# Kernel optimization log

Hardware: AMD Instinct MI355X
Metric: run time of the kernel (lower is better)

## Reference

```python
import math
import jax
import jax.numpy as jnp
import numpy as np

MUL = 32            # multiplicity of 0e and 1o in irreps_in/out
N_NODES = 50000
N_EDGES = 800000
N_BASIS = 10
N_HID = 100
NUM_NEIGHBORS = 16.0


def setup_inputs() -> dict:
    key = jax.random.key(0)
    ks = jax.random.split(key, 14)
    return {
        "node_input": jax.random.normal(ks[0], (N_NODES, 4 * MUL), jnp.float32),
        "node_attr": jnp.ones((N_NODES, 1), jnp.float32),
        "edge_src": jax.random.randint(ks[1], (N_EDGES,), 0, N_NODES, dtype=jnp.int32),
        "edge_dst": jax.random.randint(ks[2], (N_EDGES,), 0, N_NODES, dtype=jnp.int32),
        "edge_attr": jax.random.normal(ks[3], (N_EDGES, 4), jnp.float32),
        "edge_length_embedded": jax.random.uniform(ks[4], (N_EDGES, N_BASIS), dtype=jnp.float32),
        "W_sc0": jax.random.normal(ks[5], (MUL, MUL), jnp.float32),
        "W_sc1": jax.random.normal(ks[6], (MUL, MUL), jnp.float32),
        "W_l10": jax.random.normal(ks[7], (MUL, MUL), jnp.float32),
        "W_l11": jax.random.normal(ks[8], (MUL, MUL), jnp.float32),
        "W_l20": jax.random.normal(ks[9], (2 * MUL, MUL), jnp.float32),
        "W_l21": jax.random.normal(ks[10], (2 * MUL, MUL), jnp.float32),
        "W_fc1": jax.random.normal(ks[11], (N_BASIS, N_HID), jnp.float32),
        "W_fc2": jax.random.normal(ks[12], (N_HID, 4 * MUL), jnp.float32),
    }


def _fctp(x0, x1, attr, W0, W1):
    """FullyConnectedTensorProduct with a 1x0e attr: per-irrep linear * scalar attr.
    x0: [N,U], x1: [N,U,3], attr: [N,1]. Path norm alpha = 1/sqrt(fan_in)."""
    inv = 1.0 / math.sqrt(W0.shape[0])
    o0 = attr * (x0 @ W0) * inv                                    # [N,W]
    o1 = attr[:, :, None] * jnp.einsum("nud,uw->nwd", x1, W1) * inv  # [N,W,3]
    return o0, o1


def _forward(node_input, node_attr, edge_attr, edge_length_embedded,
             W_sc0, W_sc1, W_l10, W_l11, W_l20, W_l21, W_fc1, W_fc2,
             edge_src, edge_dst):
    N = node_input.shape[0]
    x0 = node_input[:, :MUL]                       # [N,32]  0e
    x1 = node_input[:, MUL:].reshape(N, MUL, 3)    # [N,32,3] 1o

    # self-connection and lin1 (both attr is scalar 0e)
    s0, s1 = _fctp(x0, x1, node_attr, W_sc0, W_sc1)
    y0, y1 = _fctp(x0, x1, node_attr, W_l10, W_l11)

    # radial MLP -> per-edge uvu weights (weight_numel = 4*MUL)
    h = jax.nn.silu(edge_length_embedded @ W_fc1 * (1.0 / math.sqrt(N_BASIS)))
    w = h @ W_fc2 * (1.0 / math.sqrt(N_HID))       # [E,128]
    w1, w2, w3, w4 = (w[:, 0*MUL:1*MUL], w[:, 1*MUL:2*MUL],
                      w[:, 2*MUL:3*MUL], w[:, 3*MUL:4*MUL])

    # gather source node features per edge
    x0s = y0[edge_src]                              # [E,32]
    x1s = y1[edge_src]                              # [E,32,3]
    ea0 = edge_attr[:, :1]                          # [E,1]   0e
    ea1 = edge_attr[:, 1:]                          # [E,3]   1o

    # segmented uvu tensor product (CG for lmax=1, component norm)
    mid0a = w1 * x0s * ea0                                         # 0e x 0e -> 0e
    mid0b = w4 * jnp.einsum("eum,em->eu", x1s, ea1) * (1.0 / math.sqrt(3.0))  # 1o x 1o -> 0e
    mid1a = (w2 * x0s)[:, :, None] * ea1[:, None, :]               # 0e x 1o -> 1o
    mid1b = w3[:, :, None] * x1s * ea0[:, None, :]                 # 1o x 0e -> 1o
    E = edge_attr.shape[0]
    edge_features = jnp.concatenate(
        [mid0a, mid0b, mid1a.reshape(E, -1), mid1b.reshape(E, -1)], axis=1)  # [E,256]

    # scatter-add to destination nodes
    agg = jax.ops.segment_sum(edge_features, edge_dst, num_segments=N)
    agg = agg * (1.0 / math.sqrt(NUM_NEIGHBORS))

    m0 = agg[:, :2 * MUL]                           # [N,64]  0e part of irreps_mid
    m1 = agg[:, 2 * MUL:].reshape(N, 2 * MUL, 3)    # [N,64,3] 1o part
    z0, z1 = _fctp(m0, m1, node_attr, W_l20, W_l21)

    # sc output_mask is all ones (every output irrep reachable)
    c_s = math.sin(math.pi / 8.0)
    c_x = math.cos(math.pi / 8.0)
    out0 = c_s * s0 + c_x * z0
    out1 = c_s * s1 + c_x * z1
    return jnp.concatenate([out0, out1.reshape(N, -1)], axis=1)   # [N,128]


def reference(node_input, node_attr, edge_src, edge_dst, edge_attr, edge_length_embedded,
              W_sc0, W_sc1, W_l10, W_l11, W_l20, W_l21, W_fc1, W_fc2):
    return _forward(node_input, node_attr, edge_attr, edge_length_embedded,
                    W_sc0, W_sc1, W_l10, W_l11, W_l20, W_l21, W_fc1, W_fc2,
                    edge_src, edge_dst)
```

## Files before the change

kernel.cpp:

```cpp
#include <hip/hip_runtime.h>
#include <hip/hip_bf16.h>

#define MUL 32
#define F4 128
#define NB 10
#define NH 100
#define EROW 136
#define FROW 72
#define REC 48

#define INV_SQRT32 0.17677669529663687f
#define INV_SQRT10 0.31622776601683794f
#define INV_SQRT100 0.1f
#define INV_SQRT3 0.5773502691896258f
#define AGG_SCALE 0.25f
#define INV8 0.125f
#define C_S 0.3826834323650898f
#define C_X 0.9238795325112867f

typedef __attribute__((ext_vector_type(8))) short short8;
typedef __attribute__((ext_vector_type(4))) float float4v;

__device__ __forceinline__ float bf2f(__hip_bfloat16 v) { return __bfloat162float(v); }
__device__ __forceinline__ unsigned short f2b(float x) {
    __hip_bfloat16 b = __float2bfloat16(x);
    return *(unsigned short*)&b;
}
__device__ __forceinline__ float b2f(unsigned short u) {
    __hip_bfloat16 b;
    *(unsigned short*)&b = u;
    return __bfloat162float(b);
}
__device__ __forceinline__ float ldin(const void* p, size_t i, int f) {
    return f ? ((const float*)p)[i] : bf2f(((const __hip_bfloat16*)p)[i]);
}

__device__ __forceinline__ void barrier_lds() {
    asm volatile("s_waitcnt lgkmcnt(0)" ::: "memory");
    __builtin_amdgcn_s_barrier();
}

__global__ void detect_dtype_kernel(const void* __restrict__ node_attr, int* __restrict__ flag) {
    unsigned w = *(const unsigned*)node_attr;
    *flag = (w == 0x3F800000u) ? 1 : 0;
}

__global__ __launch_bounds__(256) void prep_kernel(
    const void* __restrict__ Wfc1,
    const void* __restrict__ Wfc2,
    const void* __restrict__ Wl20,
    const void* __restrict__ Wl21,
    const int* __restrict__ flagp,
    unsigned short* __restrict__ w1t,
    unsigned short* __restrict__ w2t,
    unsigned short* __restrict__ w20t,
    unsigned short* __restrict__ w21t)
{
    int f = *flagp;
    int gi = blockIdx.x * 256 + threadIdx.x;
    if (gi < 128 * 128) {
        int n = gi >> 7, k = gi & 127;
        w2t[gi] = (k < NH) ? f2b(ldin(Wfc2, (size_t)k * 128 + n, f)) : 0;
    }
    if (gi < 32 * 64) {
        int v = gi >> 6, u = gi & 63;
        w20t[gi] = f2b(ldin(Wl20, (size_t)u * 32 + v, f));
        w21t[gi] = f2b(ldin(Wl21, (size_t)u * 32 + v, f));
    }
    if (gi < 112 * 32) {
        int n = gi >> 5, k = gi & 31;
        w1t[gi] = (k < NB && n < NH) ? f2b(ldin(Wfc1, (size_t)k * NH + n, f)) : 0;
    }
}

__global__ __launch_bounds__(256) void hist_kernel(
    const int* __restrict__ edst, int* __restrict__ cnt, int E)
{
    int i = blockIdx.x * 256 + threadIdx.x;
    if (i < E) atomicAdd(&cnt[edst[i]], 1);
}

__global__ __launch_bounds__(1024) void scanA_kernel(
    int* __restrict__ cnt, int* __restrict__ bsum, int N)
{
    __shared__ int wsum[16];
    int t = threadIdx.x, lane = t & 63, wid = t >> 6;
    int i = blockIdx.x * 1024 + t;
    int v = (i < N) ? cnt[i] : 0;
    int x = v;
#pragma unroll
    for (int d = 1; d < 64; d <<= 1) { int yv = __shfl_up(x, d); if (lane >= d) x += yv; }
    if (lane == 63) wsum[wid] = x;
    __syncthreads();
    if (wid == 0 && lane < 16) {
        int s = wsum[lane];
#pragma unroll
        for (int d = 1; d < 16; d <<= 1) { int yv = __shfl_up(s, d); if (lane >= d) s += yv; }
        wsum[lane] = s;
    }
    __syncthreads();
    int pre = (wid > 0 ? wsum[wid - 1] : 0);
    if (i < N) cnt[i] = pre + x - v;
    if (t == 0) bsum[blockIdx.x] = wsum[15];
}

__global__ __launch_bounds__(64) void scanB_kernel(int* __restrict__ bsum, int nb)
{
    int t = threadIdx.x;
    int carry = 0;
    for (int c0 = 0; c0 < nb; c0 += 64) {
        int idx = c0 + t;
        int v = (idx < nb) ? bsum[idx] : 0;
        int x = v;
#pragma unroll
        for (int d = 1; d < 64; d <<= 1) { int yv = __shfl_up(x, d); if (t >= d) x += yv; }
        if (idx < nb) bsum[idx] = carry + x - v;
        carry += __shfl(x, 63);
    }
}

__global__ __launch_bounds__(1024) void scanC_kernel(
    int* __restrict__ cnt, const int* __restrict__ bsum, int N)
{
    int i = blockIdx.x * 1024 + threadIdx.x;
    if (i < N) cnt[i] += bsum[blockIdx.x];
}

__global__ __launch_bounds__(256) void scatter_build_kernel(
    const int* __restrict__ edst,
    const int* __restrict__ esrc,
    const void* __restrict__ eattr,
    const void* __restrict__ ele,
    const int* __restrict__ flagp,
    int* __restrict__ cnt,
    unsigned char* __restrict__ rec, int E)
{
    int i = blockIdx.x * 256 + threadIdx.x;
    if (i >= E) return;
    int f = *flagp;
    int d = edst[i];
    int p = atomicAdd(&cnt[d], 1);

    unsigned e0 = f2b(ldin(ele, (size_t)i * NB + 0, f));
    unsigned e1 = f2b(ldin(ele, (size_t)i * NB + 1, f));
    unsigned e2 = f2b(ldin(ele, (size_t)i * NB + 2, f));
    unsigned e3 = f2b(ldin(ele, (size_t)i * NB + 3, f));
    unsigned e4 = f2b(ldin(ele, (size_t)i * NB + 4, f));
    unsigned e5 = f2b(ldin(ele, (size_t)i * NB + 5, f));
    unsigned e6 = f2b(ldin(ele, (size_t)i * NB + 6, f));
    unsigned e7 = f2b(ldin(ele, (size_t)i * NB + 7, f));
    unsigned e8 = f2b(ldin(ele, (size_t)i * NB + 8, f));
    unsigned e9 = f2b(ldin(ele, (size_t)i * NB + 9, f));
    float ea0 = ldin(eattr, (size_t)i * 4 + 0, f);
    float ea1 = ldin(eattr, (size_t)i * 4 + 1, f);
    float ea2 = ldin(eattr, (size_t)i * 4 + 2, f);
    float ea3 = ldin(eattr, (size_t)i * 4 + 3, f);

    unsigned char* r = rec + (size_t)p * REC;
    *(int4*)(r + 0)  = make_int4(esrc[i], d, (int)(e0 | (e1 << 16)), (int)(e2 | (e3 << 16)));
    *(int4*)(r + 16) = make_int4((int)(e4 | (e5 << 16)), (int)(e6 | (e7 << 16)), (int)(e8 | (e9 << 16)), 0);
    *(float4*)(r + 32) = make_float4(ea0, ea1, ea2, ea3);
}

__global__ __launch_bounds__(256) void node_y_kernel(
    const void* __restrict__ node_input,
    const void* __restrict__ node_attr,
    const void* __restrict__ Wl10,
    const void* __restrict__ Wl11,
    const int* __restrict__ flagp,
    unsigned short* __restrict__ y, int N)
{
    __shared__ float sW0[1024];
    __shared__ float sW1[1024];
    __shared__ float sX[16 * 128];
    int f = *flagp;
    int t = threadIdx.x;
    for (int i = t; i < 1024; i += 256) {
        sW0[i] = ldin(Wl10, i, f);
        sW1[i] = ldin(Wl11, i, f);
    }
    int n0 = blockIdx.x * 16;
    for (int i = t; i < 2048; i += 256) {
        int ln = i >> 7, c = i & 127, n = n0 + ln;
        sX[i] = (n < N) ? ldin(node_input, (size_t)n * F4 + c, f) : 0.f;
    }
    __syncthreads();
    for (int i = t; i < 2048; i += 256) {
        int ln = i >> 7, c = i & 127, n = n0 + ln;
        if (n >= N) continue;
        float attr = ldin(node_attr, n, f);
        float acc = 0.f;
        if (c < 32) {
#pragma unroll
            for (int u = 0; u < 32; u++) acc += sX[ln * 128 + u] * sW0[u * 32 + c];
        } else {
            int d = (c - 32) >> 5, u0 = (c - 32) & 31;
#pragma unroll
            for (int u = 0; u < 32; u++) acc += sX[ln * 128 + 32 + u * 3 + d] * sW1[u * 32 + u0];
        }
        y[(size_t)n * F4 + c] = f2b(acc * attr * INV_SQRT32);
    }
}

#define SM_ELEB  0
#define SM_HW    4096
#define SM_DST   21504
#define SM_TOTAL 21760

__global__ __launch_bounds__(256, 6) void fused_edge_kernel(
    const unsigned char* __restrict__ rec,
    const unsigned short* __restrict__ y,
    const unsigned short* __restrict__ w1t,
    const unsigned short* __restrict__ w2t,
    const unsigned short* __restrict__ w20t,
    const unsigned short* __restrict__ w21t,
    float* __restrict__ agg,
    int E)
{
    __shared__ __align__(16) char smem[SM_TOTAL];
    unsigned short* sEleB = (unsigned short*)(smem + SM_ELEB);
    unsigned short* sHW = (unsigned short*)(smem + SM_HW);
    int* sDst = (int*)(smem + SM_DST);

    int t = threadIdx.x;
    int base = blockIdx.x * 64;
    int ne = E - base;
    if (ne > 64) ne = 64;

    int w = t >> 6, lane = t & 63;
    int lm = lane & 15, quad = lane >> 4;
    int em = w * 16 + lm;

    int src = (em < ne) ? *(const int*)(rec + (size_t)(base + em) * REC) : 0;
    float4 ea4 = (em < ne) ? *(const float4*)(rec + (size_t)(base + em) * REC + 32)
                           : make_float4(0.f, 0.f, 0.f, 0.f);
    const unsigned short* yrg = y + (size_t)src * 128;
    short8 x0  = *(const short8*)(yrg + quad * 8);
    short8 xd0 = *(const short8*)(yrg + 32 + quad * 8);
    short8 xd1 = *(const short8*)(yrg + 64 + quad * 8);
    short8 xd2 = *(const short8*)(yrg + 96 + quad * 8);
    short8 w1f[7];
#pragma unroll
    for (int nt = 0; nt < 7; nt++)
        w1f[nt] = *(const short8*)(w1t + (nt * 16 + lm) * 32 + quad * 8);

    if (t < 64)
        sDst[t] = (t < ne) ? *(const int*)(rec + (size_t)(base + t) * REC + 4) : -1;
    for (int i = t; i < 64 * 32; i += 256) {
        int e = i >> 5, k = i & 31;
        unsigned short v = 0;
        if (k < NB && e < ne)
            v = *(const unsigned short*)(rec + (size_t)(base + e) * REC + 8 + 2 * k);
        sEleB[i] = v;
    }
    barrier_lds();

    {
        short8 a = *(const short8*)(sEleB + (w * 16 + lm) * 32 + quad * 8);
#pragma unroll
        for (int nt = 0; nt < 7; nt++) {
            float4v c1 = (float4v){0.f, 0.f, 0.f, 0.f};
            c1 = __builtin_amdgcn_mfma_f32_16x16x32_bf16(a, w1f[nt], c1, 0, 0, 0);
            int ch = nt * 16 + lm;
#pragma unroll
            for (int r = 0; r < 4; r++) {
                int row = w * 16 + quad * 4 + r;
                float hv = 0.f;
                if (ch < NH) {
                    float aa = c1[r] * INV_SQRT10;
                    hv = aa / (1.f + __expf(-aa));
                }
                sHW[row * EROW + ch] = f2b(hv);
            }
        }
        int e = t >> 2, seg = t & 3;
        *(uint2*)(sHW + e * EROW + 112 + seg * 4) = (uint2){0u, 0u};
    }
    barrier_lds();

    short8 hfr[4];
#pragma unroll
    for (int kc = 0; kc < 4; kc++)
        hfr[kc] = *(const short8*)(sHW + (w * 16 + lm) * EROW + kc * 32 + quad * 8);
    barrier_lds();
#pragma unroll
    for (int nt = 0; nt < 8; nt++) {
        float4v c2 = (float4v){0.f, 0.f, 0.f, 0.f};
#pragma unroll
        for (int kc = 0; kc < 4; kc++) {
            short8 b = *(const short8*)(w2t + (nt * 16 + lm) * 128 + kc * 32 + quad * 8);
            c2 = __builtin_amdgcn_mfma_f32_16x16x32_bf16(hfr[kc], b, c2, 0, 0, 0);
        }
#pragma unroll
        for (int r = 0; r < 4; r++)
            sHW[(w * 16 + quad * 4 + r) * EROW + nt * 16 + lm] = f2b(c2[r] * INV_SQRT100);
    }
    barrier_lds();

    {
        const unsigned short* wr = sHW + em * EROW;
        short8 wA = *(const short8*)(wr + quad * 8);
        short8 wB = *(const short8*)(wr + 32 + quad * 8);
        short8 wC = *(const short8*)(wr + 64 + quad * 8);
        short8 wD = *(const short8*)(wr + 96 + quad * 8);
        float ea0 = ea4.x;
        float e1x = ea4.y;
        float e1y = ea4.z;
        float e1z = ea4.w;
        float ea0S = ea0 * AGG_SCALE;
        float s3 = AGG_SCALE * INV_SQRT3;

        short8 f00, f01, f10, f11, f20, f21, f30, f31;
#pragma unroll
        for (int j = 0; j < 8; j++) {
            float x0f = b2f((unsigned short)x0[j]);
            float d0f = b2f((unsigned short)xd0[j]);
            float d1f = b2f((unsigned short)xd1[j]);
            float d2f = b2f((unsigned short)xd2[j]);
            f00[j] = (short)f2b(b2f((unsigned short)wA[j]) * x0f * ea0S);
            float tt = d0f * e1x + d1f * e1y + d2f * e1z;
            f01[j] = (short)f2b(b2f((unsigned short)wD[j]) * tt * s3);
            float p = b2f((unsigned short)wB[j]) * x0f * AGG_SCALE;
            f10[j] = (short)f2b(p * e1x);
            f20[j] = (short)f2b(p * e1y);
            f30[j] = (short)f2b(p * e1z);
            float q = b2f((unsigned short)wC[j]) * ea0S;
            f11[j] = (short)f2b(q * d0f);
            f21[j] = (short)f2b(q * d1f);
            f31[j] = (short)f2b(q * d2f);
        }

        barrier_lds();
        unsigned short* sFeatT = (unsigned short*)smem;
#pragma unroll
        for (int g = 0; g < 4; g++) {
            const unsigned short* wt = g ? w21t : w20t;
            short8 ak0 = (g == 0) ? f00 : (g == 1) ? f10 : (g == 2) ? f20 : f30;
            short8 ak1 = (g == 0) ? f01 : (g == 1) ? f11 : (g == 2) ? f21 : f31;
#pragma unroll
            for (int nt = 0; nt < 2; nt++) {
                float4v acc = (float4v){0.f, 0.f, 0.f, 0.f};
                short8 b0 = *(const short8*)(wt + (nt * 16 + lm) * 64 + quad * 8);
                short8 b1 = *(const short8*)(wt + (nt * 16 + lm) * 64 + 32 + quad * 8);
                acc = __builtin_amdgcn_mfma_f32_16x16x32_bf16(ak0, b0, acc, 0, 0, 0);
                acc = __builtin_amdgcn_mfma_f32_16x16x32_bf16(ak1, b1, acc, 0, 0, 0);
                int ch = (g == 0) ? (nt * 16 + lm) : (32 + (g - 1) * 32 + nt * 16 + lm);
                short4 sv;
                sv.x = (short)f2b(acc[0]);
                sv.y = (short)f2b(acc[1]);
                sv.z = (short)f2b(acc[2]);
                sv.w = (short)f2b(acc[3]);
                *(short4*)(sFeatT + ch * FROW + (w * 16 + quad * 4)) = sv;
            }
        }
        barrier_lds();

        if (t < 128) {
            int c = t;
            unsigned long long m =
                __ballot((lane == 0) ? 1 : (sDst[lane] != sDst[lane - 1]));
            const unsigned short* fr = sFeatT + c * FROW;
            short8 fv[8];
#pragma unroll
            for (int q8 = 0; q8 < 8; q8++)
                fv[q8] = *(const short8*)(fr + q8 * 8);
            float s = 0.f;
            int rs = 0;
#pragma unroll
            for (int e = 0; e < 64; e++) {
                s += b2f((unsigned short)fv[e >> 3][e & 7]);
                bool fl = (e == 63) || ((m >> (e + 1)) & 1ull);
                if (fl) {
                    int d = sDst[e];
                    if (d >= 0) {
                        if (rs > 0 && e < ne - 1) agg[(size_t)d * F4 + c] = s;
                        else atomicAdd(&agg[(size_t)d * F4 + c], s);
                    }
                    s = 0.f;
                    rs = e + 1;
                }
            }
        }
    }
}

__global__ __launch_bounds__(256) void out_kernel(
    const void* __restrict__ node_input,
    const void* __restrict__ node_attr,
    const void* __restrict__ Wsc0,
    const void* __restrict__ Wsc1,
    const float* __restrict__ agg,
    const int* __restrict__ flagp,
    void* __restrict__ out, int N)
{
    __shared__ float sWs0[1024], sWs1[1024];
    __shared__ float sX[16 * 128];
    __shared__ float sA[16 * 128];
    int f = *flagp;
    int t = threadIdx.x;
    for (int i = t; i < 1024; i += 256) {
        sWs0[i] = ldin(Wsc0, i, f);
        sWs1[i] = ldin(Wsc1, i, f);
    }
    int n0 = blockIdx.x * 16;
    for (int i = t; i < 2048; i += 256) {
        int ln = i >> 7, c = i & 127, n = n0 + ln;
        sX[i] = (n < N) ? ldin(node_input, (size_t)n * F4 + c, f) : 0.f;
        sA[i] = (n < N) ? agg[(size_t)n * F4 + c] : 0.f;
    }
    __syncthreads();
    for (int i = t; i < 2048; i += 256) {
        int ln = i >> 7, c = i & 127, n = n0 + ln;
        if (n >= N) continue;
        float attr = ldin(node_attr, n, f);
        float s, z;
        if (c < 32) {
            float as = 0.f;
#pragma unroll
            for (int u = 0; u < 32; u++) as += sX[ln * 128 + u] * sWs0[u * 32 + c];
            s = as * INV_SQRT32;
            z = sA[ln * 128 + c];
        } else {
            int i2 = c - 32;
            int u0 = i2 / 3, d = i2 - u0 * 3;
            float as = 0.f;
#pragma unroll
            for (int u = 0; u < 32; u++) as += sX[ln * 128 + 32 + u * 3 + d] * sWs1[u * 32 + u0];
            s = as * INV_SQRT32;
            z = sA[ln * 128 + 32 + d * 32 + u0];
        }
        float val = attr * (C_S * s + C_X * z * INV8);
        size_t oi = (size_t)n * F4 + c;
        if (f) ((float*)out)[oi] = val;
        else   ((__hip_bfloat16*)out)[oi] = __float2bfloat16(val);
    }
}

extern "C" void kernel_launch(void* const* d_in, const int* in_sizes, int n_in,
                              void* d_out, int out_size, void* d_ws, size_t ws_size,
                              hipStream_t stream) {
    const void* node_input = d_in[0];
    const void* node_attr  = d_in[1];
    const int* edge_src    = (const int*)d_in[2];
    const int* edge_dst    = (const int*)d_in[3];
    const void* edge_attr  = d_in[4];
    const void* ele        = d_in[5];
    const void* Wsc0       = d_in[6];
    const void* Wsc1       = d_in[7];
    const void* Wl10       = d_in[8];
    const void* Wl11       = d_in[9];
    const void* Wl20       = d_in[10];
    const void* Wl21       = d_in[11];
    const void* Wfc1       = d_in[12];
    const void* Wfc2       = d_in[13];

    int N = in_sizes[0] / F4;
    int E = in_sizes[2];

    char* ws = (char*)d_ws;
    int* flag = (int*)ws;
    unsigned short* y = (unsigned short*)(ws + 64);
    size_t y_b = (size_t)N * F4 * 2;
    float* agg = (float*)(ws + 64 + y_b);
    size_t agg_b = (size_t)N * F4 * 4;
    size_t off = 64 + y_b + agg_b;
    unsigned short* w2t  = (unsigned short*)(ws + off);
    unsigned short* w20t = (unsigned short*)(ws + off + 32768);
    unsigned short* w21t = (unsigned short*)(ws + off + 36864);
    unsigned short* w1t  = (unsigned short*)(ws + off + 40960);
    size_t off2 = off + 49152;
    int* cnt = (int*)(ws + off2);
    size_t cnt_b = ((size_t)N * 4 + 63) & ~(size_t)63;
    int* bsum = (int*)(ws + off2 + cnt_b);
    size_t bsum_b = 4096;
    unsigned char* rec = (unsigned char*)(ws + off2 + cnt_b + bsum_b);

    int nscan = (N + 1023) / 1024;

    detect_dtype_kernel<<<1, 1, 0, stream>>>(node_attr, flag);
    prep_kernel<<<64, 256, 0, stream>>>(Wfc1, Wfc2, Wl20, Wl21, flag, w1t, w2t, w20t, w21t);
    (void)hipMemsetAsync(cnt, 0, (size_t)N * 4, stream);
    (void)hipMemsetAsync(agg, 0, agg_b, stream);

    hist_kernel<<<(E + 255) / 256, 256, 0, stream>>>(edge_dst, cnt, E);
    scanA_kernel<<<nscan, 1024, 0, stream>>>(cnt, bsum, N);
    scanB_kernel<<<1, 64, 0, stream>>>(bsum, nscan);
    scanC_kernel<<<nscan, 1024, 0, stream>>>(cnt, bsum, N);
    scatter_build_kernel<<<(E + 255) / 256, 256, 0, stream>>>(
        edge_dst, edge_src, edge_attr, ele, flag, cnt, rec, E);

    node_y_kernel<<<(N + 15) / 16, 256, 0, stream>>>(node_input, node_attr, Wl10, Wl11, flag, y, N);

    fused_edge_kernel<<<(E + 63) / 64, 256, 0, stream>>>(
        rec, y, w1t, w2t, w20t, w21t, agg, E);

    out_kernel<<<(N + 15) / 16, 256, 0, stream>>>(node_input, node_attr, Wsc0, Wsc1,
                                                  agg, flag, d_out, N);
}
```

Before: 606.5 us.

## Use bf16 MFMA for node self-connection and lin1 linear layers

Rewrites node_y_kernel and out_kernel to compute the 32x32 per-irrep linears with 16x16x32 bf16 MFMA instructions instead of scalar FMA loops over LDS, processing 64 nodes per block. The weights are pre-transposed to bf16 once in prep_kernel, and node inputs are permuted in LDS so each 1o component forms a contiguous K slice. This removes per-block weight staging and the scalar dot-product cost, at the price of bf16 rounding of node_input and the self-connection weights, plus scattered output stores in out_kernel.

```diff
diff --git a/kernel.cpp b/kernel.cpp
--- a/kernel.cpp
+++ b/kernel.cpp
@@ -7,6 +7,7 @@
 #define NH 100
 #define EROW 136
 #define FROW 72
+#define XROW 136
 #define REC 48
 
 #define INV_SQRT32 0.17677669529663687f
@@ -17,6 +18,8 @@
 #define INV8 0.125f
 #define C_S 0.3826834323650898f
 #define C_X 0.9238795325112867f
+#define CS32 (C_S * INV_SQRT32)
+#define CX8 (C_X * INV8)
 
 typedef __attribute__((ext_vector_type(8))) short short8;
 typedef __attribute__((ext_vector_type(4))) float float4v;
@@ -50,11 +53,19 @@
     const void* __restrict__ Wfc2,
     const void* __restrict__ Wl20,
     const void* __restrict__ Wl21,
+    const void* __restrict__ Wl10,
+    const void* __restrict__ Wl11,
+    const void* __restrict__ Wsc0,
+    const void* __restrict__ Wsc1,
     const int* __restrict__ flagp,
     unsigned short* __restrict__ w1t,
     unsigned short* __restrict__ w2t,
     unsigned short* __restrict__ w20t,
-    unsigned short* __restrict__ w21t)
+    unsigned short* __restrict__ w21t,
+    unsigned short* __restrict__ w10t,
+    unsigned short* __restrict__ w11t,
+    unsigned short* __restrict__ wsc0t,
+    unsigned short* __restrict__ wsc1t)
 {
     int f = *flagp;
     int gi = blockIdx.x * 256 + threadIdx.x;
@@ -70,6 +81,13 @@
     if (gi < 112 * 32) {
         int n = gi >> 5, k = gi & 31;
         w1t[gi] = (k < NB && n < NH) ? f2b(ldin(Wfc1, (size_t)k * NH + n, f)) : 0;
+    }
+    if (gi < 1024) {
+        int c = gi >> 5, u = gi & 31;
+        w10t[gi]  = f2b(ldin(Wl10, (size_t)u * 32 + c, f));
+        w11t[gi]  = f2b(ldin(Wl11, (size_t)u * 32 + c, f));
+        wsc0t[gi] = f2b(ldin(Wsc0, (size_t)u * 32 + c, f));
+        wsc1t[gi] = f2b(ldin(Wsc1, (size_t)u * 32 + c, f));
     }
 }
 
@@ -165,40 +183,51 @@
 __global__ __launch_bounds__(256) void node_y_kernel(
     const void* __restrict__ node_input,
     const void* __restrict__ node_attr,
-    const void* __restrict__ Wl10,
-    const void* __restrict__ Wl11,
+    const unsigned short* __restrict__ w10t,
+    const unsigned short* __restrict__ w11t,
     const int* __restrict__ flagp,
     unsigned short* __restrict__ y, int N)
 {
-    __shared__ float sW0[1024];
-    __shared__ float sW1[1024];
-    __shared__ float sX[16 * 128];
+    __shared__ __align__(16) unsigned short sXp[64 * XROW];
+    __shared__ float sAt[64];
     int f = *flagp;
     int t = threadIdx.x;
-    for (int i = t; i < 1024; i += 256) {
-        sW0[i] = ldin(Wl10, i, f);
-        sW1[i] = ldin(Wl11, i, f);
-    }
-    int n0 = blockIdx.x * 16;
-    for (int i = t; i < 2048; i += 256) {
-        int ln = i >> 7, c = i & 127, n = n0 + ln;
-        sX[i] = (n < N) ? ldin(node_input, (size_t)n * F4 + c, f) : 0.f;
-    }
+    int n0 = blockIdx.x * 64;
+    for (int i = t; i < 64 * 128; i += 256) {
+        int n = i >> 7, c = i & 127;
+        float v = (n0 + n < N) ? ldin(node_input, (size_t)(n0 + n) * F4 + c, f) : 0.f;
+        int slot = (c < 32) ? c : 32 + ((c - 32) % 3) * 32 + (c - 32) / 3;
+        sXp[n * XROW + slot] = f2b(v);
+    }
+    if (t < 64) sAt[t] = (n0 + t < N) ? ldin(node_attr, n0 + t, f) : 0.f;
     __syncthreads();
-    for (int i = t; i < 2048; i += 256) {
-        int ln = i >> 7, c = i & 127, n = n0 + ln;
-        if (n >= N) continue;
-        float attr = ldin(node_attr, n, f);
-        float acc = 0.f;
-        if (c < 32) {
-#pragma unroll
-            for (int u = 0; u < 32; u++) acc += sX[ln * 128 + u] * sW0[u * 32 + c];
-        } else {
-            int d = (c - 32) >> 5, u0 = (c - 32) & 31;
-#pragma unroll
-            for (int u = 0; u < 32; u++) acc += sX[ln * 128 + 32 + u * 3 + d] * sW1[u * 32 + u0];
-        }
-        y[(size_t)n * F4 + c] = f2b(acc * attr * INV_SQRT32);
+
+    int w = t >> 6, lane = t & 63, lm = lane & 15, quad = lane >> 4;
+    int arow = (w * 16 + lm) * XROW;
+    short8 ax0 = *(const short8*)(sXp + arow + quad * 8);
+    short8 ax1[3];
+#pragma unroll
+    for (int d = 0; d < 3; d++)
+        ax1[d] = *(const short8*)(sXp + arow + 32 + d * 32 + quad * 8);
+
+#pragma unroll
+    for (int seg = 0; seg < 4; seg++) {
+        short8 a = (seg == 0) ? ax0 : ax1[seg - 1];
+        const unsigned short* wt = (seg == 0) ? w10t : w11t;
+#pragma unroll
+        for (int nt = 0; nt < 2; nt++) {
+            float4v c1 = (float4v){0.f, 0.f, 0.f, 0.f};
+            short8 b = *(const short8*)(wt + (nt * 16 + lm) * 32 + quad * 8);
+            c1 = __builtin_amdgcn_mfma_f32_16x16x32_bf16(a, b, c1, 0, 0, 0);
+#pragma unroll
+            for (int r = 0; r < 4; r++) {
+                int nl = w * 16 + quad * 4 + r;
+                int n = n0 + nl;
+                if (n < N)
+                    y[(size_t)n * F4 + seg * 32 + nt * 16 + lm] =
+                        f2b(c1[r] * sAt[nl] * INV_SQRT32);
+            }
+        }
     }
 }
 
@@ -387,52 +416,58 @@
 __global__ __launch_bounds__(256) void out_kernel(
     const void* __restrict__ node_input,
     const void* __restrict__ node_attr,
-    const void* __restrict__ Wsc0,
-    const void* __restrict__ Wsc1,
+    const unsigned short* __restrict__ wsc0t,
+    const unsigned short* __restrict__ wsc1t,
     const float* __restrict__ agg,
     const int* __restrict__ flagp,
     void* __restrict__ out, int N)
 {
-    __shared__ float sWs0[1024], sWs1[1024];
-    __shared__ float sX[16 * 128];
-    __shared__ float sA[16 * 128];
+    __shared__ __align__(16) unsigned short sXp[64 * XROW];
+    __shared__ float sAt[64];
     int f = *flagp;
     int t = threadIdx.x;
-    for (int i = t; i < 1024; i += 256) {
-        sWs0[i] = ldin(Wsc0, i, f);
-        sWs1[i] = ldin(Wsc1, i, f);
-    }
-    int n0 = blockIdx.x * 16;
-    for (int i = t; i < 2048; i += 256) {
-        int ln = i >> 7, c = i & 127, n = n0 + ln;
-        sX[i] = (n < N) ? ldin(node_input, (size_t)n * F4 + c, f) : 0.f;
-        sA[i] = (n < N) ? agg[(size_t)n * F4 + c] : 0.f;
-    }
+    int n0 = blockIdx.x * 64;
+    for (int i = t; i < 64 * 128; i += 256) {
+        int n = i >> 7, c = i & 127;
+        float v = (n0 + n < N) ? ldin(node_input, (size_t)(n0 + n) * F4 + c, f) : 0.f;
+        int slot = (c < 32) ? c : 32 + ((c - 32) % 3) * 32 + (c - 32) / 3;
+        sXp[n * XROW + slot] = f2b(v);
+    }
+    if (t < 64) sAt[t] = (n0 + t < N) ? ldin(node_attr, n0 + t, f) : 0.f;
     __syncthreads();
-    for (int i = t; i < 2048; i += 256) {
-        int ln = i >> 7, c = i & 127, n = n0 + ln;
-        if (n >= N) continue;
-        float attr = ldin(node_attr, n, f);
-        float s, z;
-        if (c < 32) {
-            float as = 0.f;
-#pragma unroll
-            for (int u = 0; u < 32; u++) as += sX[ln * 128 + u] * sWs0[u * 32 + c];
-            s = as * INV_SQRT32;
-            z = sA[ln * 128 + c];
-        } else {
-            int i2 = c - 32;
-            int u0 = i2 / 3, d = i2 - u0 * 3;
-            float as = 0.f;
-#pragma unroll
-            for (int u = 0; u < 32; u++) as += sX[ln * 128 + 32 + u * 3 + d] * sWs1[u * 32 + u0];
-            s = as * INV_SQRT32;
-            z = sA[ln * 128 + 32 + d * 32 + u0];
-        }
-        float val = attr * (C_S * s + C_X * z * INV8);
-        size_t oi = (size_t)n * F4 + c;
-        if (f) ((float*)out)[oi] = val;
-        else   ((__hip_bfloat16*)out)[oi] = __float2bfloat16(val);
+
+    int w = t >> 6, lane = t & 63, lm = lane & 15, quad = lane >> 4;
+    int arow = (w * 16 + lm) * XROW;
+    short8 ax0 = *(const short8*)(sXp + arow + quad * 8);
+    short8 ax1[3];
+#pragma unroll
+    for (int d = 0; d < 3; d++)
+        ax1[d] = *(const short8*)(sXp + arow + 32 + d * 32 + quad * 8);
+
+#pragma unroll
+    for (int seg = 0; seg < 4; seg++) {
+        short8 a = (seg == 0) ? ax0 : ax1[seg - 1];
+        const unsigned short* wt = (seg == 0) ? wsc0t : wsc1t;
+#pragma unroll
+        for (int nt = 0; nt < 2; nt++) {
+            float4v c1 = (float4v){0.f, 0.f, 0.f, 0.f};
+            short8 b = *(const short8*)(wt + (nt * 16 + lm) * 32 + quad * 8);
+            c1 = __builtin_amdgcn_mfma_f32_16x16x32_bf16(a, b, c1, 0, 0, 0);
+            int col = nt * 16 + lm;
+#pragma unroll
+            for (int r = 0; r < 4; r++) {
+                int nl = w * 16 + quad * 4 + r;
+                int n = n0 + nl;
+                if (n < N) {
+                    float z = agg[(size_t)n * F4 + seg * 32 + col];
+                    float val = sAt[nl] * (CS32 * c1[r] + CX8 * z);
+                    int c = (seg == 0) ? col : 32 + col * 3 + (seg - 1);
+                    size_t oi = (size_t)n * F4 + c;
+                    if (f) ((float*)out)[oi] = val;
+                    else   ((__hip_bfloat16*)out)[oi] = __float2bfloat16(val);
+                }
+            }
+        }
     }
 }
 
@@ -469,16 +504,23 @@
     unsigned short* w21t = (unsigned short*)(ws + off + 36864);
     unsigned short* w1t  = (unsigned short*)(ws + off + 40960);
     size_t off2 = off + 49152;
-    int* cnt = (int*)(ws + off2);
+    unsigned short* w10t  = (unsigned short*)(ws + off2);
+    unsigned short* w11t  = (unsigned short*)(ws + off2 + 2048);
+    unsigned short* wsc0t = (unsigned short*)(ws + off2 + 4096);
+    unsigned short* wsc1t = (unsigned short*)(ws + off2 + 6144);
+    size_t off3 = off2 + 8192;
+    int* cnt = (int*)(ws + off3);
     size_t cnt_b = ((size_t)N * 4 + 63) & ~(size_t)63;
-    int* bsum = (int*)(ws + off2 + cnt_b);
+    int* bsum = (int*)(ws + off3 + cnt_b);
     size_t bsum_b = 4096;
-    unsigned char* rec = (unsigned char*)(ws + off2 + cnt_b + bsum_b);
+    unsigned char* rec = (unsigned char*)(ws + off3 + cnt_b + bsum_b);
 
     int nscan = (N + 1023) / 1024;
 
     detect_dtype_kernel<<<1, 1, 0, stream>>>(node_attr, flag);
-    prep_kernel<<<64, 256, 0, stream>>>(Wfc1, Wfc2, Wl20, Wl21, flag, w1t, w2t, w20t, w21t);
+    prep_kernel<<<64, 256, 0, stream>>>(Wfc1, Wfc2, Wl20, Wl21, Wl10, Wl11, Wsc0, Wsc1,
+                                        flag, w1t, w2t, w20t, w21t,
+                                        w10t, w11t, wsc0t, wsc1t);
     (void)hipMemsetAsync(cnt, 0, (size_t)N * 4, stream);
     (void)hipMemsetAsync(agg, 0, agg_b, stream);
 
@@ -489,11 +531,12 @@
     scatter_build_kernel<<<(E + 255) / 256, 256, 0, stream>>>(
         edge_dst, edge_src, edge_attr, ele, flag, cnt, rec, E);
 
-    node_y_kernel<<<(N + 15) / 16, 256, 0, stream>>>(node_input, node_attr, Wl10, Wl11, flag, y, N);
+    node_y_kernel<<<(N + 63) / 64, 256, 0, stream>>>(node_input, node_attr,
+                                                     w10t, w11t, flag, y, N);
 
     fused_edge_kernel<<<(E + 63) / 64, 256, 0, stream>>>(
         rec, y, w1t, w2t, w20t, w21t, agg, E);
 
-    out_kernel<<<(N + 15) / 16, 256, 0, stream>>>(node_input, node_attr, Wsc0, Wsc1,
-                                                  agg, flag, d_out, N);
-}
+    out_kernel<<<(N + 63) / 64, 256, 0, stream>>>(node_input, node_attr,
+                                                  wsc0t, wsc1t, agg, flag, d_out, N);
+}
```

After: 579.4 us. 1.05x faster.
